# Optimization experiments

Measured on AMD Instinct MI355X. Metric: run time of the kernel, lower is better.

The kernel has to match this reference:

```python
import jax, jax.numpy as jnp
import numpy as np

N, E = 50000, 800000
F_IN, C1, H1 = 128, 16, 4        # conv1: 128 -> 16 per head, 4 heads (concat -> 64)
F_MID = C1 * H1                   # 64
N_CLASSES, H2 = 10, 1             # conv2: 64 -> 10, 1 head, no concat
NEG_SLOPE = 0.2


def setup_inputs() -> dict:
    key = jax.random.key(0)
    ks = jax.random.split(key, 12)
    s1 = 1.0 / np.sqrt(F_IN)
    s2 = 1.0 / np.sqrt(F_MID)
    return {
        "x": jax.random.normal(ks[0], (N, F_IN), dtype=jnp.float32),
        "edge_index": jax.random.randint(ks[1], (2, E), 0, N, dtype=jnp.int64),
        # conv1 params (GATv2: separate lin_l / lin_r, per-head attention vector, bias)
        "W1l": jax.random.normal(ks[2], (F_IN, H1 * C1), dtype=jnp.float32) * s1,
        "W1r": jax.random.normal(ks[3], (F_IN, H1 * C1), dtype=jnp.float32) * s1,
        "att1": jax.random.normal(ks[4], (H1, C1), dtype=jnp.float32) * s1,
        "b1": jnp.zeros((H1 * C1,), dtype=jnp.float32),
        # conv2 params
        "W2l": jax.random.normal(ks[5], (F_MID, H2 * N_CLASSES), dtype=jnp.float32) * s2,
        "W2r": jax.random.normal(ks[6], (F_MID, H2 * N_CLASSES), dtype=jnp.float32) * s2,
        "att2": jax.random.normal(ks[7], (H2, N_CLASSES), dtype=jnp.float32) * s2,
        "b2": jnp.zeros((N_CLASSES,), dtype=jnp.float32),
    }


def gatv2_conv(x, Wl, Wr, att, b, src, dst, concat):
    """GATv2Conv (add_self_loops=False, eval mode). src -> dst message passing."""
    H, C = att.shape
    n = x.shape[0]
    xl = (x @ Wl).reshape(n, H, C)   # source-side transform (also the value)
    xr = (x @ Wr).reshape(n, H, C)   # target-side transform
    # per-edge GATv2 score: att . LeakyReLU(xl[src] + xr[dst])
    e = jax.nn.leaky_relu(xl[src] + xr[dst], NEG_SLOPE)          # [E, H, C]
    logits = jnp.einsum("ehc,hc->eh", e, att)                    # [E, H]
    # segment softmax over incoming edges of each dst node
    m = jax.ops.segment_max(logits, dst, num_segments=n)         # [N, H]
    ex = jnp.exp(logits - m[dst])
    denom = jax.ops.segment_sum(ex, dst, num_segments=n)         # [N, H]
    alpha = ex / denom[dst]                                      # [E, H]
    out = jax.ops.segment_sum(alpha[:, :, None] * xl[src], dst, num_segments=n)  # [N, H, C]
    out = out.reshape(n, H * C) if concat else out.mean(axis=1)
    return out + b


def reference(x, edge_index, W1l, W1r, att1, b1, W2l, W2r, att2, b2):
    src, dst = edge_index[0], edge_index[1]
    h = jax.nn.elu(gatv2_conv(x, W1l, W1r, att1, b1, src, dst, concat=True))
    return gatv2_conv(h, W2l, W2r, att2, b2, src, dst, concat=False)
```

## Files before the change

### kernel.cpp

```cpp
#include <hip/hip_runtime.h>
#include <math.h>

#define NN 50000
#define NE 800000
#define FIN 128
#define NC 10
#define NEG 0.2f
#define LOG2E 1.4426950408889634f

#define NB 196
#define CHUNK 4096
#define P1B ((NE + CHUNK - 1) / CHUNK)
#define CAP 5120
#define GMT ((NN + 127) / 128)
#define LBW 200
#define WPAD 136

typedef unsigned int uint;
typedef _Float16 h2 __attribute__((ext_vector_type(2)));
typedef _Float16 h8 __attribute__((ext_vector_type(8)));
typedef float f32x4 __attribute__((ext_vector_type(4)));
typedef __fp16 hb2 __attribute__((ext_vector_type(2)));
union U2H { uint u; h2 h; };
union U4H8 { uint4 u; h8 h; };

__device__ __forceinline__ uint pkrtz_u(float a, float b) {
    union { hb2 f; uint u; } r;
    r.f = __builtin_amdgcn_cvt_pkrtz(a, b);
    return r.u;
}

__device__ __forceinline__ float dot2f(h2 a, h2 b, float c) {
#if __has_builtin(__builtin_amdgcn_fdot2)
    return __builtin_amdgcn_fdot2(a, b, c, false);
#else
    return fmaf((float)a.x, (float)b.x, fmaf((float)a.y, (float)b.y, c));
#endif
}

__device__ __forceinline__ float fexp2(float x) {
#if __has_builtin(__builtin_amdgcn_exp2f)
    return __builtin_amdgcn_exp2f(x);
#else
    return exp2f(x);
#endif
}

__device__ __forceinline__ uint ld_off(const uint* __restrict__ base, uint byteoff) {
    return *(const uint*)((const char*)base + (size_t)byteoff);
}

__device__ __forceinline__ h2 lrelu2(h2 v) {
    return __builtin_elementwise_max(v, v * (_Float16)0.2f);
}

template<int CTRL>
__device__ __forceinline__ float dpp_add(float x) {
    int y = __builtin_amdgcn_update_dpp(0, __float_as_int(x), CTRL, 0xF, 0xF, true);
    return x + __int_as_float(y);
}
__device__ __forceinline__ float red8(float t) {
    t = dpp_add<0xB1>(t);
    t = dpp_add<0x4E>(t);
    t = dpp_add<0x141>(t);
    return t;
}

__device__ __forceinline__ int excl_scan256(int v, int* sc) {
    const int t = threadIdx.x;
    sc[t] = v;
    __syncthreads();
    for (int o = 1; o < 256; o <<= 1) {
        int u = (t >= o) ? sc[t - o] : 0;
        __syncthreads();
        sc[t] += u;
        __syncthreads();
    }
    return sc[t] - v;
}


__device__ void pass1_body(const int* __restrict__ ei, uint* __restrict__ temp,
                           int* __restrict__ lbmat, char* smraw) {
    uint* pk = (uint*)smraw;
    int* h   = (int*)(smraw + 16384);
    int* h2_ = (int*)(smraw + 17408);
    int* sc  = (int*)(smraw + 18432);
    const int t = threadIdx.x;
    const int B = blockIdx.x;
    const int e0 = B * CHUNK;
    const int cnt = min(CHUNK, NE - e0);

    h[t] = 0; h2_[t] = 0;
    __syncthreads();
    for (int i = t; i < cnt; i += 256) {
        int d = ei[NE + e0 + i];
        atomicAdd(&h[d >> 8], 1);
    }
    __syncthreads();
    const int hv = h[t];
    const int ex = excl_scan256(hv, sc);
    if (t < NB) lbmat[B * LBW + t] = ex;
    if (t == NB - 1) lbmat[B * LBW + NB] = ex + hv;
    h2_[t] = ex;
    __syncthreads();
    for (int i = t; i < cnt; i += 256) {
        int s = ei[e0 + i];
        int d = ei[NE + e0 + i];
        int b = d >> 8;
        int pos = atomicAdd(&h2_[b], 1);
        pk[pos] = ((uint)s << 8) | ((uint)d & 255u);
    }
    __syncthreads();
    for (int i = t; i < cnt; i += 256) temp[B * CHUNK + i] = pk[i];
}

__device__ void gemm1_body(const float* __restrict__ x,
                           const float* __restrict__ W1l,
                           const float* __restrict__ W1r,
                           _Float16* __restrict__ xlh,
                           _Float16* __restrict__ xrh,
                           int n0, char* smraw) {
    _Float16 (*WtL)[WPAD] = (_Float16(*)[WPAD])smraw;
    _Float16 (*WtR)[WPAD] = (_Float16(*)[WPAD])(smraw + 64 * WPAD * 2);
    const int t = threadIdx.x;

    for (int i = t; i < FIN * 64; i += 256) {
        int k = i >> 6, c = i & 63;
        WtL[c][k] = (_Float16)W1l[i];
        WtR[c][k] = (_Float16)W1r[i];
    }
    __syncthreads();

    const int lane = t & 63;
    const int wid = t >> 6;
    const int col16 = lane & 15;
    const int kgrp = (lane >> 4) * 8;

    f32x4 acc[2][8] = {};
    for (int kk = 0; kk < FIN; kk += 32) {
        U4H8 a[2];
#pragma unroll
        for (int s = 0; s < 2; ++s) {
            int arow = n0 + s * 64 + wid * 16 + col16;
            if (arow < NN) {
                const float4* xp = (const float4*)(x + (size_t)arow * FIN + kk + kgrp);
                float4 v0 = xp[0], v1 = xp[1];
                a[s].u = make_uint4(pkrtz_u(v0.x, v0.y), pkrtz_u(v0.z, v0.w),
                                    pkrtz_u(v1.x, v1.y), pkrtz_u(v1.z, v1.w));
            } else {
                a[s].u = make_uint4(0u, 0u, 0u, 0u);
            }
        }
        const int kof = kk + kgrp;
#pragma unroll
        for (int ct = 0; ct < 4; ++ct) {
            U4H8 b; b.u = *(const uint4*)&WtL[ct * 16 + col16][kof];
            acc[0][ct] = __builtin_amdgcn_mfma_f32_16x16x32_f16(a[0].h, b.h, acc[0][ct], 0, 0, 0);
            acc[1][ct] = __builtin_amdgcn_mfma_f32_16x16x32_f16(a[1].h, b.h, acc[1][ct], 0, 0, 0);
        }
#pragma unroll
        for (int ct = 0; ct < 4; ++ct) {
            U4H8 b; b.u = *(const uint4*)&WtR[ct * 16 + col16][kof];
            acc[0][4 + ct] = __builtin_amdgcn_mfma_f32_16x16x32_f16(a[0].h, b.h, acc[0][4 + ct], 0, 0, 0);
            acc[1][4 + ct] = __builtin_amdgcn_mfma_f32_16x16x32_f16(a[1].h, b.h, acc[1][4 + ct], 0, 0, 0);
        }
    }
#pragma unroll
    for (int s = 0; s < 2; ++s) {
        const int crow0 = n0 + s * 64 + wid * 16 + (lane >> 4) * 4;
#pragma unroll
        for (int ct = 0; ct < 8; ++ct) {
            _Float16* __restrict__ op = (ct < 4) ? xlh : xrh;
            const int col = (ct & 3) * 16 + col16;
#pragma unroll
            for (int r = 0; r < 4; ++r) {
                int node = crow0 + r;
                if (node < NN) op[(size_t)node * 64 + col] = (_Float16)acc[s][ct][r];
            }
        }
    }
}

__global__ __launch_bounds__(256) void k_fusedA(const float* __restrict__ x,
                                                const int* __restrict__ ei,
                                                const float* __restrict__ W1l,
                                                const float* __restrict__ W1r,
                                                _Float16* __restrict__ xlh,
                                                _Float16* __restrict__ xrh,
                                                uint* __restrict__ temp,
                                                int* __restrict__ lbmat) {
    __shared__ __align__(16) char smraw[64 * WPAD * 2 * 2];
    if (blockIdx.x < P1B) {
        pass1_body(ei, temp, lbmat, smraw);
    } else {
        int g = blockIdx.x - P1B;
        gemm1_body(x, W1l, W1r, xlh, xrh, g * 128, smraw);
    }
}


__global__ __launch_bounds__(256) void k_pass2(const uint* __restrict__ temp,
                                               const int* __restrict__ lbmat,
                                               int* __restrict__ rowptr,
                                               int* __restrict__ deg,
                                               int* __restrict__ csr_src) {
    __shared__ uint P[CAP];
    __shared__ int nh[256], nbx[256], ncur[256], sc[256];
    const int t = threadIdx.x;
    const int b = blockIdx.x;

    int lbv = 0, len = 0;
    if (t < P1B) {
        lbv = lbmat[t * LBW + b];
        len = lbmat[t * LBW + b + 1] - lbv;
    }
    const int colstart = excl_scan256(len, sc);
    __syncthreads();
    const int cnt = sc[255];
    __syncthreads();
    (void)excl_scan256(lbv, sc);
    __syncthreads();
    const int csrbase = sc[255];
    __syncthreads();
    nh[t] = 0; ncur[t] = 0;
    __syncthreads();
    if (t < P1B) {
        const uint* src = temp + t * CHUNK + lbv;
        for (int i = 0; i < len; ++i) P[colstart + i] = src[i];
    }
    __syncthreads();
    for (int i = t; i < cnt; i += 256) atomicAdd(&nh[P[i] & 255u], 1);
    __syncthreads();
    const int c = nh[t];
    const int nb_ex = excl_scan256(c, sc);
    nbx[t] = nb_ex;
    const int gnode = b * 256 + t;
    if (gnode < NN) { rowptr[gnode] = csrbase + nb_ex; deg[gnode] = c; }
    __syncthreads();
    for (int i = t; i < cnt; i += 256) {
        uint v = P[i];
        int l = (int)(v & 255u);
        int r = atomicAdd(&ncur[l], 1);
        csr_src[csrbase + nbx[l] + r] = (int)(v >> 8);
    }
}


__global__ __launch_bounds__(256) void k_agg1(const uint* __restrict__ xlh2,
                                              const uint* __restrict__ xrh2,
                                              const int* __restrict__ rowptr,
                                              const int* __restrict__ deg,
                                              const int* __restrict__ csr_src,
                                              const float* __restrict__ att1,
                                              const float* __restrict__ b1,
                                              uint* __restrict__ hbh2) {
    const int node = blockIdx.x * 4 + (threadIdx.x >> 6);
    if (node >= NN) return;
    const int lane = threadIdx.x & 63;
    const int fl = lane & 31;
    const uint fl4 = (uint)fl * 4u;
    const int hid = lane >> 5;
    float2 av = *(const float2*)&att1[2 * fl];
    U2H att; att.u = pkrtz_u(av.x * LOG2E, av.y * LOG2E);
    U2H xrf; xrf.u = xrh2[(size_t)node * 32 + fl];
    const int start = rowptr[node];
    const int dg = deg[node];
    const int permbase = (lane & 32) >> 3;

    float denom = 0.f, acc0 = 0.f, acc1 = 0.f;
    for (int base = 0; base < dg; base += 64) {
        int idx = base + lane;
        uint srcb = (idx < dg) ? ((uint)csr_src[start + idx] << 7) : 0u;
        int rem = dg - base; if (rem > 64) rem = 64;
        int iters = (rem + 1) >> 1;
        int thr = (rem - hid + 1) >> 1;
        for (int jj = 0; jj < iters; jj += 4) {
            uint o0 = (uint)__builtin_amdgcn_ds_bpermute((jj + 0) * 8 + permbase, (int)srcb) + fl4;
            uint o1 = (uint)__builtin_amdgcn_ds_bpermute((jj + 1) * 8 + permbase, (int)srcb) + fl4;
            uint o2 = (uint)__builtin_amdgcn_ds_bpermute((jj + 2) * 8 + permbase, (int)srcb) + fl4;
            uint o3 = (uint)__builtin_amdgcn_ds_bpermute((jj + 3) * 8 + permbase, (int)srcb) + fl4;
            U2H v0; v0.u = ld_off(xlh2, o0);
            U2H v1; v1.u = ld_off(xlh2, o1);
            U2H v2; v2.u = ld_off(xlh2, o2);
            U2H v3; v3.u = ld_off(xlh2, o3);
            float t0 = red8(dot2f(lrelu2(v0.h + xrf.h), att.h, 0.f));
            float t1 = red8(dot2f(lrelu2(v1.h + xrf.h), att.h, 0.f));
            float t2 = red8(dot2f(lrelu2(v2.h + xrf.h), att.h, 0.f));
            float t3 = red8(dot2f(lrelu2(v3.h + xrf.h), att.h, 0.f));
            float e0 = (jj + 0 < thr) ? fexp2(t0) : 0.f;
            float e1 = (jj + 1 < thr) ? fexp2(t1) : 0.f;
            float e2 = (jj + 2 < thr) ? fexp2(t2) : 0.f;
            float e3 = (jj + 3 < thr) ? fexp2(t3) : 0.f;
            denom += (e0 + e1) + (e2 + e3);
            acc0 = fmaf(e0, (float)v0.h.x, acc0);
            acc0 = fmaf(e1, (float)v1.h.x, acc0);
            acc0 = fmaf(e2, (float)v2.h.x, acc0);
            acc0 = fmaf(e3, (float)v3.h.x, acc0);
            acc1 = fmaf(e0, (float)v0.h.y, acc1);
            acc1 = fmaf(e1, (float)v1.h.y, acc1);
            acc1 = fmaf(e2, (float)v2.h.y, acc1);
            acc1 = fmaf(e3, (float)v3.h.y, acc1);
        }
    }
    denom += __shfl_xor(denom, 32);
    acc0  += __shfl_xor(acc0, 32);
    acc1  += __shfl_xor(acc1, 32);
    if (lane < 32) {
        float r = (dg > 0) ? (1.0f / denom) : 0.f;
        float2 bv = *(const float2*)&b1[2 * fl];
        float o0 = fmaf(acc0, r, bv.x);
        float o1 = fmaf(acc1, r, bv.y);
        o0 = o0 > 0.f ? o0 : expm1f(o0);
        o1 = o1 > 0.f ? o1 : expm1f(o1);
        hbh2[(size_t)node * 32 + fl] = pkrtz_u(o0, o1);
    }
}


__global__ __launch_bounds__(256) void k_gemm2(const uint* __restrict__ hbh2,
                                               const float* __restrict__ W2l,
                                               const float* __restrict__ W2r,
                                               uint* __restrict__ xl2h,
                                               uint* __restrict__ xr2h) {
    int n = blockIdx.x * 256 + threadIdx.x;
    if (n >= NN) return;
    float al[NC] = {}, ar[NC] = {};
    const uint4* hr4 = (const uint4*)(hbh2 + (size_t)n * 32);
#pragma unroll
    for (int q = 0; q < 8; ++q) {
        uint4 qq = hr4[q];
        uint uu[4] = {qq.x, qq.y, qq.z, qq.w};
#pragma unroll
        for (int j = 0; j < 4; ++j) {
            U2H hh; hh.u = uu[j];
            float f0 = (float)hh.h.x, f1 = (float)hh.h.y;
            int k = q * 8 + j * 2;
            const float* wl0 = W2l + k * NC;
            const float* wr0 = W2r + k * NC;
#pragma unroll
            for (int c = 0; c < NC; ++c) {
                al[c] = fmaf(f0, wl0[c], fmaf(f1, wl0[NC + c], al[c]));
                ar[c] = fmaf(f0, wr0[c], fmaf(f1, wr0[NC + c], ar[c]));
            }
        }
    }
    uint p0 = pkrtz_u(al[0], al[1]);
    uint p1 = pkrtz_u(al[2], al[3]);
    uint p2 = pkrtz_u(al[4], al[5]);
    uint p3 = pkrtz_u(al[6], al[7]);
    uint p4 = pkrtz_u(al[8], al[9]);
    *(uint4*)&xl2h[(size_t)n * 8]     = make_uint4(p0, p1, p2, p3);
    *(uint4*)&xl2h[(size_t)n * 8 + 4] = make_uint4(p4, 0u, 0u, 0u);
    p0 = pkrtz_u(ar[0], ar[1]);
    p1 = pkrtz_u(ar[2], ar[3]);
    p2 = pkrtz_u(ar[4], ar[5]);
    p3 = pkrtz_u(ar[6], ar[7]);
    p4 = pkrtz_u(ar[8], ar[9]);
    *(uint4*)&xr2h[(size_t)n * 8]     = make_uint4(p0, p1, p2, p3);
    *(uint4*)&xr2h[(size_t)n * 8 + 4] = make_uint4(p4, 0u, 0u, 0u);
}


__global__ __launch_bounds__(256) void k_agg2(const uint* __restrict__ xl2h,
                                              const uint* __restrict__ xr2h,
                                              const int* __restrict__ rowptr,
                                              const int* __restrict__ deg,
                                              const int* __restrict__ csr_src,
                                              const float* __restrict__ att2,
                                              const float* __restrict__ b2,
                                              float* __restrict__ out) {
    const int node = blockIdx.x * 4 + (threadIdx.x >> 6);
    if (node >= NN) return;
    const int lane = threadIdx.x & 63;
    const int fp = lane & 7;
    const uint fp4 = (uint)fp * 4u;
    const int eg = lane >> 3;
    U2H att;
    if (fp < 5) {
        float2 av = *(const float2*)&att2[2 * fp];
        att.u = pkrtz_u(av.x * LOG2E, av.y * LOG2E);
    } else {
        att.u = 0;
    }
    U2H xrf; xrf.u = xr2h[(size_t)node * 8 + fp];
    const int start = rowptr[node];
    const int dg = deg[node];
    const int permbase = eg * 4;

    float denom = 0.f, acc0 = 0.f, acc1 = 0.f;
    for (int base = 0; base < dg; base += 64) {
        int idx = base + lane;
        uint srcb = (idx < dg) ? ((uint)csr_src[start + idx] << 5) : 0u;
        int rem = dg - base; if (rem > 64) rem = 64;
        int iters = (rem + 7) >> 3;
        int thr = (rem - eg + 7) >> 3;
        for (int jj = 0; jj < iters; jj += 4) {
            uint o[4]; U2H v[4];
#pragma unroll
            for (int k = 0; k < 4; ++k)
                o[k] = (uint)__builtin_amdgcn_ds_bpermute((jj + k) * 32 + permbase, (int)srcb) + fp4;
#pragma unroll
            for (int k = 0; k < 4; ++k)
                v[k].u = ld_off(xl2h, o[k]);
#pragma unroll
            for (int k = 0; k < 4; ++k) {
                float tl = red8(dot2f(lrelu2(v[k].h + xrf.h), att.h, 0.f));
                float e = (jj + k < thr) ? fexp2(tl) : 0.f;
                denom += e;
                acc0 = fmaf(e, (float)v[k].h.x, acc0);
                acc1 = fmaf(e, (float)v[k].h.y, acc1);
            }
        }
    }
#pragma unroll
    for (int m = 8; m <= 32; m <<= 1) {
        denom += __shfl_xor(denom, m);
        acc0  += __shfl_xor(acc0, m);
        acc1  += __shfl_xor(acc1, m);
    }
    if (lane < 5) {
        float r = (dg > 0) ? (1.0f / denom) : 0.f;
        float2 o;
        o.x = fmaf(acc0, r, b2[2 * fp]);
        o.y = fmaf(acc1, r, b2[2 * fp + 1]);
        *(float2*)&out[(size_t)node * NC + 2 * fp] = o;
    }
}


extern "C" void kernel_launch(void* const* d_in, const int* in_sizes, int n_in,
                              void* d_out, int out_size, void* d_ws, size_t ws_size,
                              hipStream_t stream) {
    const float* x    = (const float*)d_in[0];
    const int*   ei   = (const int*)d_in[1];
    const float* W1l  = (const float*)d_in[2];
    const float* W1r  = (const float*)d_in[3];
    const float* att1 = (const float*)d_in[4];
    const float* b1   = (const float*)d_in[5];
    const float* W2l  = (const float*)d_in[6];
    const float* W2r  = (const float*)d_in[7];
    const float* att2 = (const float*)d_in[8];
    const float* b2   = (const float*)d_in[9];
    float* out = (float*)d_out;

    char* w = (char*)d_ws;
    size_t off = 0;
    auto alloc = [&](size_t bytes) -> void* {
        void* p = w + off;
        off = (off + bytes + 255) & ~(size_t)255;
        return p;
    };
    uint* xlh2   = (uint*)alloc((size_t)NN * 32 * 4);
    uint* xrh2   = (uint*)alloc((size_t)NN * 32 * 4);
    uint* hbh2   = (uint*)alloc((size_t)NN * 32 * 4);
    uint* xl2h   = (uint*)alloc((size_t)NN * 8 * 4);
    uint* xr2h   = (uint*)alloc((size_t)NN * 8 * 4);
    uint* temp   = (uint*)alloc((size_t)P1B * CHUNK * 4);
    int*  lbmat  = (int*)alloc((size_t)P1B * LBW * 4);
    int*  rowptr = (int*)alloc((size_t)NN * 4);
    int*  deg    = (int*)alloc((size_t)NN * 4);
    int*  csr_src = (int*)alloc((size_t)(NE + 64) * 4);

    k_fusedA<<<P1B + GMT, 256, 0, stream>>>(x, ei, W1l, W1r,
                                            (_Float16*)xlh2, (_Float16*)xrh2,
                                            temp, lbmat);
    k_pass2<<<NB, 256, 0, stream>>>(temp, lbmat, rowptr, deg, csr_src);
    k_agg1<<<(NN + 3) / 4, 256, 0, stream>>>(xlh2, xrh2, rowptr, deg, csr_src, att1, b1, hbh2);
    k_gemm2<<<(NN + 255) / 256, 256, 0, stream>>>(hbh2, W2l, W2r, xl2h, xr2h);
    k_agg2<<<(NN + 3) / 4, 256, 0, stream>>>(xl2h, xr2h, rowptr, deg, csr_src, att2, b2, out);
}
```

Baseline: 92.94 us.

## Split GEMM1 tiles across fused kernels to overlap with CSR pass2

The layer-1 GEMM tiles are split in two. The first 196 tiles stay fused with pass1, and the rest run inside a new fused kernel alongside the pass2 CSR-building blocks. This balances work between the two launches so that pass2, which uses few blocks, overlaps with GEMM work instead of running alone. The pass2 copy loop is also unrolled by 8 to expose more memory-level parallelism. Shared memory is reused through a raw buffer, which is large enough for pass2's 24KB.

```diff
diff --git a/kernel.cpp b/kernel.cpp
--- a/kernel.cpp
+++ b/kernel.cpp
@@ -13,6 +13,8 @@
 #define P1B ((NE + CHUNK - 1) / CHUNK)
 #define CAP 5120
 #define GMT ((NN + 127) / 128)
+#define GH1 196
+#define GH2 (GMT - GH1)
 #define LBW 200
 #define WPAD 136
 
@@ -115,6 +117,66 @@
     for (int i = t; i < cnt; i += 256) temp[B * CHUNK + i] = pk[i];
 }
 
+
+__device__ void pass2_body(const uint* __restrict__ temp,
+                           const int* __restrict__ lbmat,
+                           int* __restrict__ rowptr,
+                           int* __restrict__ deg,
+                           int* __restrict__ csr_src,
+                           int b, char* smraw) {
+    uint* P   = (uint*)smraw;
+    int* nh   = (int*)(smraw + 20480);
+    int* nbx  = (int*)(smraw + 21504);
+    int* ncur = (int*)(smraw + 22528);
+    int* sc   = (int*)(smraw + 23552);
+    const int t = threadIdx.x;
+
+    int lbv = 0, len = 0;
+    if (t < P1B) {
+        lbv = lbmat[t * LBW + b];
+        len = lbmat[t * LBW + b + 1] - lbv;
+    }
+    const int colstart = excl_scan256(len, sc);
+    __syncthreads();
+    const int cnt = sc[255];
+    __syncthreads();
+    (void)excl_scan256(lbv, sc);
+    __syncthreads();
+    const int csrbase = sc[255];
+    __syncthreads();
+    nh[t] = 0; ncur[t] = 0;
+    __syncthreads();
+    if (t < P1B) {
+        const uint* src = temp + t * CHUNK + lbv;
+        int i = 0;
+        for (; i + 8 <= len; i += 8) {
+            uint r0 = src[i + 0], r1 = src[i + 1], r2 = src[i + 2], r3 = src[i + 3];
+            uint r4 = src[i + 4], r5 = src[i + 5], r6 = src[i + 6], r7 = src[i + 7];
+            P[colstart + i + 0] = r0; P[colstart + i + 1] = r1;
+            P[colstart + i + 2] = r2; P[colstart + i + 3] = r3;
+            P[colstart + i + 4] = r4; P[colstart + i + 5] = r5;
+            P[colstart + i + 6] = r6; P[colstart + i + 7] = r7;
+        }
+        for (; i < len; ++i) P[colstart + i] = src[i];
+    }
+    __syncthreads();
+    for (int i = t; i < cnt; i += 256) atomicAdd(&nh[P[i] & 255u], 1);
+    __syncthreads();
+    const int c = nh[t];
+    const int nb_ex = excl_scan256(c, sc);
+    nbx[t] = nb_ex;
+    const int gnode = b * 256 + t;
+    if (gnode < NN) { rowptr[gnode] = csrbase + nb_ex; deg[gnode] = c; }
+    __syncthreads();
+    for (int i = t; i < cnt; i += 256) {
+        uint v = P[i];
+        int l = (int)(v & 255u);
+        int r = atomicAdd(&ncur[l], 1);
+        csr_src[csrbase + nbx[l] + r] = (int)(v >> 8);
+    }
+}
+
+
 __device__ void gemm1_body(const float* __restrict__ x,
                            const float* __restrict__ W1l,
                            const float* __restrict__ W1r,
@@ -181,6 +243,7 @@
         }
     }
 }
+
 
 __global__ __launch_bounds__(256) void k_fusedA(const float* __restrict__ x,
                                                 const int* __restrict__ ei,
@@ -200,49 +263,22 @@
 }
 
 
-__global__ __launch_bounds__(256) void k_pass2(const uint* __restrict__ temp,
-                                               const int* __restrict__ lbmat,
-                                               int* __restrict__ rowptr,
-                                               int* __restrict__ deg,
-                                               int* __restrict__ csr_src) {
-    __shared__ uint P[CAP];
-    __shared__ int nh[256], nbx[256], ncur[256], sc[256];
-    const int t = threadIdx.x;
-    const int b = blockIdx.x;
-
-    int lbv = 0, len = 0;
-    if (t < P1B) {
-        lbv = lbmat[t * LBW + b];
-        len = lbmat[t * LBW + b + 1] - lbv;
-    }
-    const int colstart = excl_scan256(len, sc);
-    __syncthreads();
-    const int cnt = sc[255];
-    __syncthreads();
-    (void)excl_scan256(lbv, sc);
-    __syncthreads();
-    const int csrbase = sc[255];
-    __syncthreads();
-    nh[t] = 0; ncur[t] = 0;
-    __syncthreads();
-    if (t < P1B) {
-        const uint* src = temp + t * CHUNK + lbv;
-        for (int i = 0; i < len; ++i) P[colstart + i] = src[i];
-    }
-    __syncthreads();
-    for (int i = t; i < cnt; i += 256) atomicAdd(&nh[P[i] & 255u], 1);
-    __syncthreads();
-    const int c = nh[t];
-    const int nb_ex = excl_scan256(c, sc);
-    nbx[t] = nb_ex;
-    const int gnode = b * 256 + t;
-    if (gnode < NN) { rowptr[gnode] = csrbase + nb_ex; deg[gnode] = c; }
-    __syncthreads();
-    for (int i = t; i < cnt; i += 256) {
-        uint v = P[i];
-        int l = (int)(v & 255u);
-        int r = atomicAdd(&ncur[l], 1);
-        csr_src[csrbase + nbx[l] + r] = (int)(v >> 8);
+__global__ __launch_bounds__(256) void k_fusedB(const float* __restrict__ x,
+                                                const float* __restrict__ W1l,
+                                                const float* __restrict__ W1r,
+                                                _Float16* __restrict__ xlh,
+                                                _Float16* __restrict__ xrh,
+                                                const uint* __restrict__ temp,
+                                                const int* __restrict__ lbmat,
+                                                int* __restrict__ rowptr,
+                                                int* __restrict__ deg,
+                                                int* __restrict__ csr_src) {
+    __shared__ __align__(16) char smraw[64 * WPAD * 2 * 2];
+    if (blockIdx.x < NB) {
+        pass2_body(temp, lbmat, rowptr, deg, csr_src, blockIdx.x, smraw);
+    } else {
+        int g = GH1 + (blockIdx.x - NB);
+        gemm1_body(x, W1l, W1r, xlh, xrh, g * 128, smraw);
     }
 }
 
@@ -462,10 +498,12 @@
     int*  deg    = (int*)alloc((size_t)NN * 4);
     int*  csr_src = (int*)alloc((size_t)(NE + 64) * 4);
 
-    k_fusedA<<<P1B + GMT, 256, 0, stream>>>(x, ei, W1l, W1r,
+    k_fusedA<<<P1B + GH1, 256, 0, stream>>>(x, ei, W1l, W1r,
                                             (_Float16*)xlh2, (_Float16*)xrh2,
                                             temp, lbmat);
-    k_pass2<<<NB, 256, 0, stream>>>(temp, lbmat, rowptr, deg, csr_src);
+    k_fusedB<<<NB + GH2, 256, 0, stream>>>(x, W1l, W1r,
+                                           (_Float16*)xlh2, (_Float16*)xrh2,
+                                           temp, lbmat, rowptr, deg, csr_src);
     k_agg1<<<(NN + 3) / 4, 256, 0, stream>>>(xlh2, xrh2, rowptr, deg, csr_src, att1, b1, hbh2);
     k_gemm2<<<(NN + 255) / 256, 256, 0, stream>>>(hbh2, W2l, W2r, xl2h, xr2h);
     k_agg2<<<(NN + 3) / 4, 256, 0, stream>>>(xl2h, xr2h, rowptr, deg, csr_src, att2, b2, out);
```

After: 107.7 us. 1.16x slower.
